# Optimization experiments

Measured on AMD Instinct MI355X. Metric: run time of the kernel, lower is better.

Reference implementation:

```python
import jax, jax.numpy as jnp
import numpy as np

N, E, D, L, RBF = 20000, 320000, 128, 3, 64
CUTOFF = 5.0
LN_EPS = 1e-5


def setup_inputs() -> dict:
    key = jax.random.key(0)
    ks = jax.random.split(key, 20)
    s = 0.05
    inp = {
        'z': jax.random.normal(ks[0], (N, 64), jnp.float32),
        'pos': jax.random.normal(ks[1], (N, 3), jnp.float32),
        'edge_index': jax.random.randint(ks[2], (2, E), 0, N),
        'in_w': jax.random.normal(ks[3], (64, D), jnp.float32) * s,
        'in_b': jnp.zeros((D,), jnp.float32),
        'filt_w': jax.random.normal(ks[4], (RBF, 3 * D), jnp.float32) * s,
        'filt_b': jnp.zeros((3 * D,), jnp.float32),
        'inter_w1': jax.random.normal(ks[5], (L, D, D), jnp.float32) * s,
        'inter_b1': jnp.zeros((L, D), jnp.float32),
        'inter_w2': jax.random.normal(ks[6], (L, D, 3 * D), jnp.float32) * s,
        'inter_b2': jnp.zeros((L, 3 * D), jnp.float32),
        'mix_mu_w': jax.random.normal(ks[7], (L, D, 2 * D), jnp.float32) * s,
        'mix_w1': jax.random.normal(ks[8], (L, 2 * D, D), jnp.float32) * s,
        'mix_b1': jnp.zeros((L, D), jnp.float32),
        'mix_w2': jax.random.normal(ks[9], (L, D, 3 * D), jnp.float32) * s,
        'mix_b2': jnp.zeros((L, 3 * D), jnp.float32),
        'mu_proj_w': jnp.zeros((D,), jnp.float32),  # nn.init.constant_(0.0) in source
        'ln_g': jnp.ones((D,), jnp.float32),
        'ln_b': jnp.zeros((D,), jnp.float32),
    }
    return inp


def painn_forward(z, pos, in_w, in_b, filt_w, filt_b, inter_w1, inter_b1,
                  inter_w2, inter_b2, mix_mu_w, mix_w1, mix_b1, mix_w2, mix_b2,
                  mu_proj_w, ln_g, ln_b, edge_index):
    idx_i, idx_j = edge_index[0], edge_index[1]
    # edge geometry
    r_ij = pos[idx_j] - pos[idx_i]                               # [E,3]
    d_ij = jnp.maximum(jnp.linalg.norm(r_ij, axis=1, keepdims=True), 1e-8)  # [E,1]
    dir_ij = r_ij / d_ij                                          # [E,3]
    # gaussian smearing
    offset = jnp.linspace(0.0, CUTOFF, RBF).astype(jnp.float32)
    coeff = -0.5 / (offset[1] - offset[0]) ** 2
    phi = jnp.exp(coeff * (d_ij - offset) ** 2)                   # [E,RBF]
    # cosine cutoff
    xc = jnp.clip(d_ij / CUTOFF, 0.0, 1.0)
    fcut = 0.5 * (jnp.cos(jnp.pi * xc) + 1.0) * (xc < 1.0)        # [E,1]
    filters = (phi @ filt_w + filt_b) * fcut                      # [E,3D]
    filters = jnp.clip(jnp.nan_to_num(filters), -5.0, 5.0)
    Wij = filters[:, None, :]                                     # [E,1,3D]

    q = jax.nn.silu(z @ in_w + in_b)[:, None, :]                  # [N,1,D]
    mu = jnp.zeros((N, 3, D), q.dtype)                            # [N,3,D]

    for l in range(L):
        # interaction (edge gather -> gate -> scatter-add)
        x = jax.nn.silu(q @ inter_w1[l] + inter_b1[l]) @ inter_w2[l] + inter_b2[l]  # [N,1,3D]
        xj = x[idx_j] * Wij                                       # [E,1,3D]
        dq, dmuR, dmumu = jnp.split(xj, 3, axis=-1)               # each [E,1,D]
        muj = mu[idx_j]                                           # [E,3,D]
        q = q + jax.ops.segment_sum(dq, idx_i, num_segments=N)
        dmu = dmuR * dir_ij[:, :, None] + dmumu * muj             # [E,3,D]
        mu = mu + jax.ops.segment_sum(dmu, idx_i, num_segments=N)
        # intra-atomic mixing
        mu_mix = mu @ mix_mu_w[l]                                  # [N,3,2D]
        mu_V, mu_W = jnp.split(mu_mix, 2, axis=-1)                 # [N,3,D]
        mu_Vn = jnp.sqrt(jnp.sum(mu_V ** 2, axis=-2, keepdims=True) + 1e-8)  # [N,1,D]
        ctx = jnp.concatenate([q, mu_Vn], axis=-1)                 # [N,1,2D]
        xm = jax.nn.silu(ctx @ mix_w1[l] + mix_b1[l]) @ mix_w2[l] + mix_b2[l]  # [N,1,3D]
        dq_i, dmu_i, dqmu_i = jnp.split(xm, 3, axis=-1)
        q = q + dq_i + dqmu_i * jnp.sum(mu_V * mu_W, axis=1, keepdims=True)
        mu = mu + dmu_i * mu_W

    node_attr = jnp.clip(jnp.nan_to_num(q[:, 0, :]), -5.0, 5.0)   # [N,D]
    mean = jnp.mean(node_attr, axis=-1, keepdims=True)
    var = jnp.var(node_attr, axis=-1, keepdims=True)
    node_attr = (node_attr - mean) * jax.lax.rsqrt(var + LN_EPS) * ln_g + ln_b
    node_attr = jnp.nan_to_num(jnp.tanh(node_attr))

    mu = jnp.nan_to_num(mu)
    mu_node = jax.ops.segment_sum(mu[idx_j], idx_i, num_segments=N)  # [N,3,D]
    mu_node = jnp.clip(jnp.nan_to_num(mu_node), -5.0, 5.0)
    pos_attr = jnp.clip(jnp.nan_to_num(mu_node @ mu_proj_w), -5.0, 5.0)  # [N,3]
    return node_attr, pos_attr


def reference(z, pos, edge_index, in_w, in_b, filt_w, filt_b, inter_w1, inter_b1,
              inter_w2, inter_b2, mix_mu_w, mix_w1, mix_b1, mix_w2, mix_b2,
              mu_proj_w, ln_g, ln_b):
    return painn_forward(z, pos, in_w, in_b, filt_w, filt_b, inter_w1, inter_b1,
                         inter_w2, inter_b2, mix_mu_w, mix_w1, mix_b1, mix_w2,
                         mix_b2, mu_proj_w, ln_g, ln_b, edge_index)
```

## Files before the change

kernel.cpp:

```cpp
#include <hip/hip_runtime.h>
#include <math.h>

#ifndef M_PI
#define M_PI 3.14159265358979323846
#endif

static constexpr int N_NODES = 20000;
static constexpr int N_EDGES = 320000;
static constexpr int NLAYER  = 3;
static constexpr int NB_SCAN = (N_NODES + 255) / 256;
static constexpr int TAB_T   = 1024;

typedef _Float16 f16;
typedef __attribute__((ext_vector_type(2))) _Float16 f16x2;
typedef __attribute__((ext_vector_type(8))) _Float16 f16x8;
typedef __attribute__((ext_vector_type(4))) float f32x4;

__global__ void k_hist(const int* __restrict__ idx_i, int* __restrict__ cnt) {
  int e = blockIdx.x * 256 + threadIdx.x;
  if (e < N_EDGES) atomicAdd(&cnt[idx_i[e]], 1);
}

__global__ void k_scan_blk(const int* __restrict__ cnt, int* __restrict__ incl,
                           int* __restrict__ bsum) {
  __shared__ int buf[256];
  int t = threadIdx.x;
  int i = blockIdx.x * 256 + t;
  int v = (i < N_NODES) ? cnt[i] : 0;
  buf[t] = v;
  __syncthreads();
  #pragma unroll
  for (int off = 1; off < 256; off <<= 1) {
    int x = (t >= off) ? buf[t - off] : 0;
    __syncthreads();
    buf[t] += x;
    __syncthreads();
  }
  if (i < N_NODES) incl[i] = buf[t];
  if (t == 255) bsum[blockIdx.x] = buf[255];
}

__global__ void k_scan_top(int* __restrict__ bsum) {
  __shared__ int buf[128];
  int t = threadIdx.x;
  int v = (t < NB_SCAN) ? bsum[t] : 0;
  buf[t] = v;
  __syncthreads();
  #pragma unroll
  for (int off = 1; off < 128; off <<= 1) {
    int x = (t >= off) ? buf[t - off] : 0;
    __syncthreads();
    buf[t] += x;
    __syncthreads();
  }
  if (t <= NB_SCAN) bsum[t] = buf[t] - v;
}

__global__ void k_scan_add(const int* __restrict__ cnt, const int* __restrict__ incl,
                           const int* __restrict__ bsum, int* __restrict__ rs,
                           int* __restrict__ cur) {
  int i = blockIdx.x * 256 + threadIdx.x;
  if (i < N_NODES) {
    int v = bsum[blockIdx.x] + incl[i] - cnt[i];
    rs[i] = v;
    cur[i] = v;
  }
  if (i == 0) rs[N_NODES] = bsum[NB_SCAN];
}

__global__ void k_fill_geom(const int* __restrict__ idx_all, const float* __restrict__ pos,
                            int* __restrict__ cur, float4* __restrict__ geo,
                            int* __restrict__ jperm) {
  int e = blockIdx.x * 256 + threadIdx.x;
  if (e >= N_EDGES) return;
  int i = idx_all[e];
  int j = idx_all[N_EDGES + e];
  int p = atomicAdd(&cur[i], 1);
  float rx = pos[j*3+0] - pos[i*3+0];
  float ry = pos[j*3+1] - pos[i*3+1];
  float rz = pos[j*3+2] - pos[i*3+2];
  float d = sqrtf(rx*rx + ry*ry + rz*rz);
  d = fmaxf(d, 1e-8f);
  float inv = 1.0f / d;
  geo[p] = make_float4(d, rx*inv, ry*inv, rz*inv);
  jperm[p] = j;
}

struct WJob { const float* src; f16* dst; int kshift; int ld; int col0; int nk; };
struct WJobs { WJob j[16]; };

__global__ __launch_bounds__(256) void k_prep(WJobs jb, const float* __restrict__ filt_w,
                                              const float* __restrict__ filt_b,
                                              f16* __restrict__ tab) {
  if (blockIdx.y < 16) {
    WJob w = jb.j[blockIdx.y];
    int t = blockIdx.x * 256 + threadIdx.x;
    if (t >= w.nk) return;
    int K = 1 << w.kshift;
    int n = t >> w.kshift;
    int k = t & (K - 1);
    w.dst[t] = (f16)w.src[(size_t)k * w.ld + w.col0 + n];
    return;
  }
  if (blockIdx.x >= 128) return;
  const int t = (blockIdx.y - 16) * 128 + blockIdx.x;
  __shared__ float ph[64];
  const int tid = threadIdx.x;
  const float dist = 5.0f * (float)t / (float)(TAB_T - 1);
  const float delta = 5.0f / 63.0f;
  const float coeff = -0.5f / (delta * delta);
  if (tid < 64) {
    float u = dist - delta * (float)tid;
    ph[tid] = expf(coeff * u * u);
  }
  __syncthreads();
  float xc = dist * 0.2f;
  float fc = (xc < 1.0f) ? 0.5f * (cosf((float)M_PI * xc) + 1.0f) : 0.0f;
  for (int n = tid; n < 384; n += 256) {
    float acc = 0.f;
    #pragma unroll
    for (int k = 0; k < 64; ++k) acc += ph[k] * filt_w[k * 384 + n];
    float v = (acc + filt_b[n]) * fc;
    v = fminf(fmaxf(v, -5.0f), 5.0f);
    tab[(size_t)t * 384 + n] = (f16)v;
  }
}

__global__ __launch_bounds__(256) void k_embed_i(
    const float* __restrict__ z, const f16* __restrict__ Win, const float* __restrict__ bin,
    const f16* __restrict__ Wi1, const float* __restrict__ bi1,
    const f16* __restrict__ Wi2, const float* __restrict__ bi2,
    float* __restrict__ q, f16* __restrict__ xout) {
  __shared__ __align__(16) char pool[16896];
  f16* QS  = (f16*)pool;
  f16* H2S = (f16*)(pool + 8448);
  const int tid = threadIdx.x;
  const int wave = tid >> 6, lane = tid & 63;
  const int lr = lane & 15, lk = lane >> 4;
  const int wmB = (wave & 1) * 16, wnB = (wave >> 1) * 64;
  const int n0 = blockIdx.x * 32;

  f32x4 accP[4] = {};
  #pragma unroll
  for (int kk = 0; kk < 2; ++kk) {
    const float* zp = z + (size_t)(n0 + wmB + lr) * 64 + kk * 32 + lk * 8;
    float4 v0 = ((const float4*)zp)[0];
    float4 v1 = ((const float4*)zp)[1];
    f16x8 af;
    af[0]=(f16)v0.x; af[1]=(f16)v0.y; af[2]=(f16)v0.z; af[3]=(f16)v0.w;
    af[4]=(f16)v1.x; af[5]=(f16)v1.y; af[6]=(f16)v1.z; af[7]=(f16)v1.w;
    f16x8 bf[4];
    #pragma unroll
    for (int nt = 0; nt < 4; ++nt)
      bf[nt] = *(const f16x8*)&Win[(size_t)(wnB + nt * 16 + lr) * 64 + kk * 32 + lk * 8];
    #pragma unroll
    for (int nt = 0; nt < 4; ++nt)
      accP[nt] = __builtin_amdgcn_mfma_f32_16x16x32_f16(af, bf[nt], accP[nt], 0, 0, 0);
  }
  #pragma unroll
  for (int nt = 0; nt < 4; ++nt) {
    int col = wnB + nt * 16 + lr;
    float bv = bin[col];
    #pragma unroll
    for (int rr = 0; rr < 4; ++rr) {
      int row = wmB + lk * 4 + rr;
      float v = accP[nt][rr] + bv;
      v = v / (1.0f + expf(-v));
      q[(size_t)(n0 + row) * 128 + col] = v;
      QS[row * 132 + col] = (f16)v;
    }
  }
  __syncthreads();

  f32x4 accD[4] = {};
  #pragma unroll
  for (int kk = 0; kk < 4; ++kk) {
    f16x8 af = *(const f16x8*)&QS[(wmB + lr) * 132 + kk * 32 + lk * 8];
    f16x8 bf[4];
    #pragma unroll
    for (int nt = 0; nt < 4; ++nt)
      bf[nt] = *(const f16x8*)&Wi1[(size_t)(wnB + nt * 16 + lr) * 128 + kk * 32 + lk * 8];
    #pragma unroll
    for (int nt = 0; nt < 4; ++nt)
      accD[nt] = __builtin_amdgcn_mfma_f32_16x16x32_f16(af, bf[nt], accD[nt], 0, 0, 0);
  }
  #pragma unroll
  for (int nt = 0; nt < 4; ++nt) {
    int col = wnB + nt * 16 + lr;
    float bv = bi1[col];
    #pragma unroll
    for (int rr = 0; rr < 4; ++rr) {
      int row = wmB + lk * 4 + rr;
      float v = accD[nt][rr] + bv;
      v = v / (1.0f + expf(-v));
      H2S[row * 132 + col] = (f16)v;
    }
  }
  __syncthreads();

  #pragma unroll
  for (int cc = 0; cc < 3; ++cc) {
    f32x4 accE[4] = {};
    #pragma unroll
    for (int kk = 0; kk < 4; ++kk) {
      f16x8 af = *(const f16x8*)&H2S[(wmB + lr) * 132 + kk * 32 + lk * 8];
      f16x8 bf[4];
      #pragma unroll
      for (int nt = 0; nt < 4; ++nt)
        bf[nt] = *(const f16x8*)&Wi2[(size_t)(cc * 128 + wnB + nt * 16 + lr) * 128 + kk * 32 + lk * 8];
      #pragma unroll
      for (int nt = 0; nt < 4; ++nt)
        accE[nt] = __builtin_amdgcn_mfma_f32_16x16x32_f16(af, bf[nt], accE[nt], 0, 0, 0);
    }
    #pragma unroll
    for (int nt = 0; nt < 4; ++nt) {
      int gn = cc * 128 + wnB + nt * 16 + lr;
      float bv = bi2[gn];
      #pragma unroll
      for (int rr = 0; rr < 4; ++rr) {
        int gm = n0 + wmB + lk * 4 + rr;
        xout[(size_t)gm * 384 + gn] = (f16)(accE[nt][rr] + bv);
      }
    }
  }
}

template<int MODE>
__global__ __launch_bounds__(256) void k_mix(
    float* __restrict__ q, f16* __restrict__ mu,
    const f16* __restrict__ Wmu,
    const f16* __restrict__ W1, const float* __restrict__ b1,
    const f16* __restrict__ W2, const float* __restrict__ b2,
    const f16* __restrict__ Wi1, const float* __restrict__ bi1,
    const f16* __restrict__ Wi2, const float* __restrict__ bi2,
    f16* __restrict__ xout,
    const float* __restrict__ ln_g, const float* __restrict__ ln_b,
    float* __restrict__ out_node) {
  __shared__ __align__(16) char pool[50688 + 25344];
  f16*   MM  = (f16*)pool;
  char*  scr = pool + 50688;
  f16*   As4 = (f16*)scr;
  f16*   VN  = (f16*)scr;
  f16*   HS  = (f16*)(scr + 8448);
  f16*   QS  = (f16*)(scr + 16896);
  f16*   H2S = (f16*)scr;
  float* QSf = (float*)scr;

  const int tid = threadIdx.x;
  const int wave = tid >> 6, lane = tid & 63;
  const int lr = lane & 15, lk = lane >> 4;
  const int n0 = blockIdx.x * 32;
  const int r0 = n0 * 3;

  #pragma unroll
  for (int rep = 0; rep < 6; ++rep) {
    int idx = rep * 256 + tid;
    int row = idx >> 4;
    int g   = idx & 15;
    int kb = g >> 2, c8 = g & 3;
    f16x8 v = *(const f16x8*)(mu + (size_t)(r0 + row) * 128 + g * 8);
    *(f16x8*)&As4[((kb * 96 + row) << 5) + ((c8 ^ ((row >> 1) & 3)) << 3)] = v;
  }
  __syncthreads();

  const int wmA = (wave & 1) * 48;
  const int wnA0 = (wave >> 1) * 64;
  #pragma unroll
  for (int half = 0; half < 2; ++half) {
    f32x4 accA[3][4] = {};
    #pragma unroll
    for (int kk = 0; kk < 4; ++kk) {
      f16x8 af[3], bf[4];
      #pragma unroll
      for (int mt = 0; mt < 3; ++mt) {
        int r = wmA + mt * 16 + lr;
        af[mt] = *(const f16x8*)&As4[((kk * 96 + r) << 5) + ((lk ^ ((r >> 1) & 3)) << 3)];
      }
      #pragma unroll
      for (int nt = 0; nt < 4; ++nt)
        bf[nt] = *(const f16x8*)&Wmu[(size_t)(half * 128 + wnA0 + nt * 16 + lr) * 128 + kk * 32 + lk * 8];
      #pragma unroll
      for (int mt = 0; mt < 3; ++mt)
        #pragma unroll
        for (int nt = 0; nt < 4; ++nt)
          accA[mt][nt] = __builtin_amdgcn_mfma_f32_16x16x32_f16(af[mt], bf[nt], accA[mt][nt], 0, 0, 0);
    }
    #pragma unroll
    for (int mt = 0; mt < 3; ++mt)
      #pragma unroll
      for (int nt = 0; nt < 4; ++nt) {
        int col = half * 128 + wnA0 + nt * 16 + lr;
        #pragma unroll
        for (int rr = 0; rr < 4; ++rr) {
          int row = wmA + mt * 16 + lk * 4 + rr;
          MM[row * 264 + col] = (f16)accA[mt][nt][rr];
        }
      }
  }
  __syncthreads();

  #pragma unroll
  for (int rep = 0; rep < 16; ++rep) {
    int idx = rep * 256 + tid;
    int nn = idx >> 7, c = idx & 127;
    float V0 = (float)MM[(nn * 3 + 0) * 264 + c];
    float V1 = (float)MM[(nn * 3 + 1) * 264 + c];
    float V2 = (float)MM[(nn * 3 + 2) * 264 + c];
    float vnv = sqrtf(V0 * V0 + V1 * V1 + V2 * V2 + 1e-8f);
    int kb = c >> 5, c8 = (c >> 3) & 3, ce = c & 7;
    VN[((kb * 32 + nn) << 5) + ((c8 ^ ((nn >> 1) & 3)) << 3) + ce] = (f16)vnv;
  }
  __syncthreads();

  const int wmB = (wave & 1) * 16, wnB = (wave >> 1) * 64;
  f32x4 accB[4] = {};
  #pragma unroll
  for (int kk = 0; kk < 8; ++kk) {
    f16x8 af;
    int row = wmB + lr;
    if (kk < 4) {
      const float* qp_ = q + (size_t)(n0 + row) * 128 + kk * 32 + lk * 8;
      float4 v0 = ((const float4*)qp_)[0];
      float4 v1 = ((const float4*)qp_)[1];
      af[0]=(f16)v0.x; af[1]=(f16)v0.y; af[2]=(f16)v0.z; af[3]=(f16)v0.w;
      af[4]=(f16)v1.x; af[5]=(f16)v1.y; af[6]=(f16)v1.z; af[7]=(f16)v1.w;
    } else {
      af = *(const f16x8*)&VN[(((kk - 4) * 32 + row) << 5) + ((lk ^ ((row >> 1) & 3)) << 3)];
    }
    f16x8 bf[4];
    #pragma unroll
    for (int nt = 0; nt < 4; ++nt)
      bf[nt] = *(const f16x8*)&W1[(size_t)(wnB + nt * 16 + lr) * 256 + kk * 32 + lk * 8];
    #pragma unroll
    for (int nt = 0; nt < 4; ++nt)
      accB[nt] = __builtin_amdgcn_mfma_f32_16x16x32_f16(af, bf[nt], accB[nt], 0, 0, 0);
  }
  #pragma unroll
  for (int nt = 0; nt < 4; ++nt) {
    int col = wnB + nt * 16 + lr;
    float bv = b1[col];
    #pragma unroll
    for (int rr = 0; rr < 4; ++rr) {
      int row = wmB + lk * 4 + rr;
      float v = accB[nt][rr] + bv;
      v = v / (1.0f + expf(-v));
      HS[row * 132 + col] = (f16)v;
    }
  }
  __syncthreads();

  f32x4 accC[3][4] = {};
  #pragma unroll
  for (int cc = 0; cc < 3; ++cc)
    #pragma unroll
    for (int kk = 0; kk < 4; ++kk) {
      f16x8 af = *(const f16x8*)&HS[(wmB + lr) * 132 + kk * 32 + lk * 8];
      f16x8 bf[4];
      #pragma unroll
      for (int nt = 0; nt < 4; ++nt)
        bf[nt] = *(const f16x8*)&W2[(size_t)(cc * 128 + wnB + nt * 16 + lr) * 128 + kk * 32 + lk * 8];
      #pragma unroll
      for (int nt = 0; nt < 4; ++nt)
        accC[cc][nt] = __builtin_amdgcn_mfma_f32_16x16x32_f16(af, bf[nt], accC[cc][nt], 0, 0, 0);
    }
  __syncthreads();

  #pragma unroll
  for (int nt = 0; nt < 4; ++nt) {
    int col = wnB + nt * 16 + lr;
    float b_dq = b2[col], b_dmu = b2[128 + col], b_dqmu = b2[256 + col];
    #pragma unroll
    for (int rr = 0; rr < 4; ++rr) {
      int nn = wmB + lk * 4 + rr;
      int gm = n0 + nn;
      float dq   = accC[0][nt][rr] + b_dq;
      float dmu  = accC[1][nt][rr] + b_dmu;
      float dqmu = accC[2][nt][rr] + b_dqmu;
      float V0 = (float)MM[(nn * 3 + 0) * 264 + col], W0 = (float)MM[(nn * 3 + 0) * 264 + 128 + col];
      float V1 = (float)MM[(nn * 3 + 1) * 264 + col], W1v = (float)MM[(nn * 3 + 1) * 264 + 128 + col];
      float V2 = (float)MM[(nn * 3 + 2) * 264 + col], W2v = (float)MM[(nn * 3 + 2) * 264 + 128 + col];
      float svw = V0 * W0 + V1 * W1v + V2 * W2v;
      size_t qi = (size_t)gm * 128 + col;
      float qnew = q[qi] + dq + dqmu * svw;
      if constexpr (MODE == 0) {
        q[qi] = qnew;
        QS[nn * 132 + col] = (f16)qnew;
      } else {
        QSf[nn * 132 + col] = qnew;
      }
      f16* mr = mu + (size_t)gm * 384;
      mr[col]       = (f16)((float)mr[col]       + dmu * W0);
      mr[128 + col] = (f16)((float)mr[128 + col] + dmu * W1v);
      mr[256 + col] = (f16)((float)mr[256 + col] + dmu * W2v);
    }
  }
  __syncthreads();

  if constexpr (MODE == 0) {
    f32x4 accD[4] = {};
    #pragma unroll
    for (int kk = 0; kk < 4; ++kk) {
      f16x8 af = *(const f16x8*)&QS[(wmB + lr) * 132 + kk * 32 + lk * 8];
      f16x8 bf[4];
      #pragma unroll
      for (int nt = 0; nt < 4; ++nt)
        bf[nt] = *(const f16x8*)&Wi1[(size_t)(wnB + nt * 16 + lr) * 128 + kk * 32 + lk * 8];
      #pragma unroll
      for (int nt = 0; nt < 4; ++nt)
        accD[nt] = __builtin_amdgcn_mfma_f32_16x16x32_f16(af, bf[nt], accD[nt], 0, 0, 0);
    }
    #pragma unroll
    for (int nt = 0; nt < 4; ++nt) {
      int col = wnB + nt * 16 + lr;
      float bv = bi1[col];
      #pragma unroll
      for (int rr = 0; rr < 4; ++rr) {
        int row = wmB + lk * 4 + rr;
        float v = accD[nt][rr] + bv;
        v = v / (1.0f + expf(-v));
        H2S[row * 132 + col] = (f16)v;
      }
    }
    __syncthreads();
    #pragma unroll
    for (int cc = 0; cc < 3; ++cc) {
      f32x4 accE[4] = {};
      #pragma unroll
      for (int kk = 0; kk < 4; ++kk) {
        f16x8 af = *(const f16x8*)&H2S[(wmB + lr) * 132 + kk * 32 + lk * 8];
        f16x8 bf[4];
        #pragma unroll
        for (int nt = 0; nt < 4; ++nt)
          bf[nt] = *(const f16x8*)&Wi2[(size_t)(cc * 128 + wnB + nt * 16 + lr) * 128 + kk * 32 + lk * 8];
        #pragma unroll
        for (int nt = 0; nt < 4; ++nt)
          accE[nt] = __builtin_amdgcn_mfma_f32_16x16x32_f16(af, bf[nt], accE[nt], 0, 0, 0);
      }
      #pragma unroll
      for (int nt = 0; nt < 4; ++nt) {
        int gn = cc * 128 + wnB + nt * 16 + lr;
        float bv = bi2[gn];
        #pragma unroll
        for (int rr = 0; rr < 4; ++rr) {
          int gm = n0 + wmB + lk * 4 + rr;
          xout[(size_t)gm * 384 + gn] = (f16)(accE[nt][rr] + bv);
        }
      }
    }
  } else {
    const int d0 = lane * 2;
    #pragma unroll
    for (int rr2 = 0; rr2 < 8; ++rr2) {
      int nn = wave * 8 + rr2;
      float v0 = QSf[nn * 132 + d0];
      float v1 = QSf[nn * 132 + d0 + 1];
      v0 = fminf(fmaxf(v0, -5.f), 5.f);
      v1 = fminf(fmaxf(v1, -5.f), 5.f);
      float s = v0 + v1, s2 = v0 * v0 + v1 * v1;
      #pragma unroll
      for (int off = 32; off > 0; off >>= 1) {
        s  += __shfl_down(s,  off, 64);
        s2 += __shfl_down(s2, off, 64);
      }
      s  = __shfl(s,  0, 64);
      s2 = __shfl(s2, 0, 64);
      float mean = s * (1.0f / 128.0f);
      float var  = s2 * (1.0f / 128.0f) - mean * mean;
      float r = rsqrtf(var + 1e-5f);
      size_t o = (size_t)(n0 + nn) * 128 + d0;
      out_node[o]     = tanhf((v0 - mean) * r * ln_g[d0]     + ln_b[d0]);
      out_node[o + 1] = tanhf((v1 - mean) * r * ln_g[d0 + 1] + ln_b[d0 + 1]);
    }
  }
}

template<bool HASMU>
__global__ __launch_bounds__(256) void k_edge_msg(
    const int* __restrict__ rs, const int* __restrict__ jperm,
    const f16* __restrict__ x, const f16* __restrict__ tab,
    const float4* __restrict__ geo, const f16* __restrict__ mu_in,
    float* __restrict__ q, f16* __restrict__ mu_out) {
  const int wid  = threadIdx.x >> 6;
  const int lane = threadIdx.x & 63;
  const int i = blockIdx.x * 4 + wid;
  if (i >= N_NODES) return;
  const int d0 = lane * 2;
  const float scale = (float)(TAB_T - 1) / 5.0f;
  float aqx = 0.f, aqy = 0.f;
  float a0x = 0.f, a0y = 0.f, a1x = 0.f, a1y = 0.f, a2x = 0.f, a2y = 0.f;
  const int s = rs[i], e = rs[i + 1];

  for (int p = s; p < e; ++p) {
    int j = jperm[p];
    float4 g = geo[p];
    float u = fminf(g.x, 5.0f) * scale;
    int t0 = min((int)u, TAB_T - 2);
    float fr = u - (float)t0, fo = 1.0f - fr;
    const f16* ta = tab + (size_t)t0 * 384;
    const f16* xj = x + (size_t)j * 384;
    f16x2 ta0 = *(const f16x2*)(ta + d0);
    f16x2 ta1 = *(const f16x2*)(ta + 128 + d0);
    f16x2 tb0 = *(const f16x2*)(ta + 384 + d0);
    f16x2 tb1 = *(const f16x2*)(ta + 512 + d0);
    f16x2 xv0 = *(const f16x2*)(xj + d0);
    f16x2 xv1 = *(const f16x2*)(xj + 128 + d0);
    float W0x = fo * (float)ta0[0] + fr * (float)tb0[0];
    float W0y = fo * (float)ta0[1] + fr * (float)tb0[1];
    float W1x = fo * (float)ta1[0] + fr * (float)tb1[0];
    float W1y = fo * (float)ta1[1] + fr * (float)tb1[1];
    float m1x = (float)xv1[0] * W1x, m1y = (float)xv1[1] * W1y;
    aqx = fmaf((float)xv0[0], W0x, aqx);
    aqy = fmaf((float)xv0[1], W0y, aqy);
    if constexpr (HASMU) {
      f16x2 ta2 = *(const f16x2*)(ta + 256 + d0);
      f16x2 tb2 = *(const f16x2*)(ta + 640 + d0);
      f16x2 xv2 = *(const f16x2*)(xj + 256 + d0);
      const f16* mj = mu_in + (size_t)j * 384;
      f16x2 mv0 = *(const f16x2*)(mj + d0);
      f16x2 mv1 = *(const f16x2*)(mj + 128 + d0);
      f16x2 mv2 = *(const f16x2*)(mj + 256 + d0);
      float W2x = fo * (float)ta2[0] + fr * (float)tb2[0];
      float W2y = fo * (float)ta2[1] + fr * (float)tb2[1];
      float m2x = (float)xv2[0] * W2x, m2y = (float)xv2[1] * W2y;
      a0x += m1x * g.y + m2x * (float)mv0[0];
      a0y += m1y * g.y + m2y * (float)mv0[1];
      a1x += m1x * g.z + m2x * (float)mv1[0];
      a1y += m1y * g.z + m2y * (float)mv1[1];
      a2x += m1x * g.w + m2x * (float)mv2[0];
      a2y += m1y * g.w + m2y * (float)mv2[1];
    } else {
      a0x += m1x * g.y; a0y += m1y * g.y;
      a1x += m1x * g.z; a1y += m1y * g.z;
      a2x += m1x * g.w; a2y += m1y * g.w;
    }
  }

  float* qp = q + (size_t)i * 128 + d0;
  float2 qv = *(float2*)qp;
  qv.x += aqx; qv.y += aqy;
  *(float2*)qp = qv;
  f16* mout = mu_out + (size_t)i * 384;
  f16x2 o0, o1, o2;
  if constexpr (HASMU) {
    const f16* min_ = mu_in + (size_t)i * 384;
    f16x2 i0 = *(const f16x2*)(min_ + d0);
    f16x2 i1 = *(const f16x2*)(min_ + 128 + d0);
    f16x2 i2 = *(const f16x2*)(min_ + 256 + d0);
    o0[0] = (f16)((float)i0[0] + a0x); o0[1] = (f16)((float)i0[1] + a0y);
    o1[0] = (f16)((float)i1[0] + a1x); o1[1] = (f16)((float)i1[1] + a1y);
    o2[0] = (f16)((float)i2[0] + a2x); o2[1] = (f16)((float)i2[1] + a2y);
  } else {
    o0[0] = (f16)a0x; o0[1] = (f16)a0y;
    o1[0] = (f16)a1x; o1[1] = (f16)a1y;
    o2[0] = (f16)a2x; o2[1] = (f16)a2y;
  }
  *(f16x2*)(mout + d0)       = o0;
  *(f16x2*)(mout + 128 + d0) = o1;
  *(f16x2*)(mout + 256 + d0) = o2;
}

__global__ __launch_bounds__(256) void k_posattr(
    const int* __restrict__ rs, const int* __restrict__ jperm,
    const f16* __restrict__ mu, const float* __restrict__ w, float* __restrict__ pos_out) {
  const int wid  = threadIdx.x >> 6;
  const int lane = threadIdx.x & 63;
  const int i = blockIdx.x * 4 + wid;
  if (i >= N_NODES) return;
  const int d0 = lane * 2;
  float a0x = 0.f, a0y = 0.f, a1x = 0.f, a1y = 0.f, a2x = 0.f, a2y = 0.f;
  float wx = w[d0], wy = w[d0 + 1];
  if (wx != 0.0f || wy != 0.0f) {
    const int s = rs[i], e = rs[i + 1];
    for (int p = s; p < e; ++p) {
      int j = jperm[p];
      const f16* mj = mu + (size_t)j * 384;
      f16x2 A0 = *(const f16x2*)(mj + d0);
      f16x2 A1 = *(const f16x2*)(mj + 128 + d0);
      f16x2 A2 = *(const f16x2*)(mj + 256 + d0);
      a0x += (float)A0[0]; a0y += (float)A0[1];
      a1x += (float)A1[0]; a1y += (float)A1[1];
      a2x += (float)A2[0]; a2y += (float)A2[1];
    }
  }
  float s0 = fminf(fmaxf(a0x, -5.f), 5.f) * wx + fminf(fmaxf(a0y, -5.f), 5.f) * wy;
  float s1 = fminf(fmaxf(a1x, -5.f), 5.f) * wx + fminf(fmaxf(a1y, -5.f), 5.f) * wy;
  float s2 = fminf(fmaxf(a2x, -5.f), 5.f) * wx + fminf(fmaxf(a2y, -5.f), 5.f) * wy;
  #pragma unroll
  for (int off = 32; off > 0; off >>= 1) {
    s0 += __shfl_down(s0, off, 64);
    s1 += __shfl_down(s1, off, 64);
    s2 += __shfl_down(s2, off, 64);
  }
  if (lane == 0) {
    pos_out[(size_t)i * 3 + 0] = fminf(fmaxf(s0, -5.f), 5.f);
    pos_out[(size_t)i * 3 + 1] = fminf(fmaxf(s1, -5.f), 5.f);
    pos_out[(size_t)i * 3 + 2] = fminf(fmaxf(s2, -5.f), 5.f);
  }
}

extern "C" void kernel_launch(void* const* d_in, const int* in_sizes, int n_in,
                              void* d_out, int out_size, void* d_ws, size_t ws_size,
                              hipStream_t stream) {
  const float* z         = (const float*)d_in[0];
  const float* pos       = (const float*)d_in[1];
  const int*   edge_idx  = (const int*)d_in[2];
  const float* in_w      = (const float*)d_in[3];
  const float* in_b      = (const float*)d_in[4];
  const float* filt_w    = (const float*)d_in[5];
  const float* filt_b    = (const float*)d_in[6];
  const float* inter_w1  = (const float*)d_in[7];
  const float* inter_b1  = (const float*)d_in[8];
  const float* inter_w2  = (const float*)d_in[9];
  const float* inter_b2  = (const float*)d_in[10];
  const float* mix_mu_w  = (const float*)d_in[11];
  const float* mix_w1    = (const float*)d_in[12];
  const float* mix_b1    = (const float*)d_in[13];
  const float* mix_w2    = (const float*)d_in[14];
  const float* mix_b2    = (const float*)d_in[15];
  const float* mu_proj_w = (const float*)d_in[16];
  const float* ln_g      = (const float*)d_in[17];
  const float* ln_b      = (const float*)d_in[18];

  char* base = (char*)d_ws;
  size_t off = 0;
  auto alloc = [&](size_t bytes) -> char* {
    char* p = base + off;
    off += (bytes + 255) & ~(size_t)255;
    return p;
  };
  float*  q     = (float*)alloc((size_t)N_NODES * 128 * 4);
  f16*    x16   = (f16*)alloc((size_t)N_NODES * 384 * 2);
  f16*    mu_a  = (f16*)alloc((size_t)N_NODES * 384 * 2);
  f16*    mu_b  = (f16*)alloc((size_t)N_NODES * 384 * 2);
  float4* geo   = (float4*)alloc((size_t)N_EDGES * 16);
  int*    cnt   = (int*)alloc((size_t)N_NODES * 4);
  int*    incl  = (int*)alloc((size_t)N_NODES * 4);
  int*    bsum  = (int*)alloc(128 * 4);
  int*    rs    = (int*)alloc((size_t)(N_NODES + 1) * 4);
  int*    cur   = (int*)alloc((size_t)N_NODES * 4);
  int*    jperm = (int*)alloc((size_t)N_EDGES * 4);
  f16*    tab   = (f16*)alloc((size_t)TAB_T * 384 * 2);
  f16* wt_in = (f16*)alloc((size_t)128 * 64 * 2);
  f16* wt_i1 = (f16*)alloc((size_t)3 * 128 * 128 * 2);
  f16* wt_i2 = (f16*)alloc((size_t)3 * 384 * 128 * 2);
  f16* wt_mu = (f16*)alloc((size_t)3 * 256 * 128 * 2);
  f16* wt_x1 = (f16*)alloc((size_t)3 * 128 * 256 * 2);
  f16* wt_x2 = (f16*)alloc((size_t)3 * 384 * 128 * 2);
  if (off > ws_size) return;

  float* out_node = (float*)d_out;
  float* out_pos  = (float*)d_out + (size_t)N_NODES * 128;

  {
    WJobs jb;
    int ji = 0;
    jb.j[ji++] = {in_w, wt_in, 6, 128, 0, 128 * 64};
    for (int l = 0; l < 3; ++l)
      jb.j[ji++] = {inter_w1 + (size_t)l*128*128, wt_i1 + (size_t)l*128*128, 7, 128, 0, 128*128};
    for (int l = 0; l < 3; ++l)
      jb.j[ji++] = {inter_w2 + (size_t)l*128*384, wt_i2 + (size_t)l*384*128, 7, 384, 0, 384*128};
    for (int l = 0; l < 3; ++l)
      jb.j[ji++] = {mix_mu_w + (size_t)l*128*256, wt_mu + (size_t)l*256*128, 7, 256, 0, 256*128};
    for (int l = 0; l < 3; ++l)
      jb.j[ji++] = {mix_w1 + (size_t)l*256*128, wt_x1 + (size_t)l*128*256, 8, 128, 0, 128*256};
    for (int l = 0; l < 3; ++l)
      jb.j[ji++] = {mix_w2 + (size_t)l*128*384, wt_x2 + (size_t)l*384*128, 7, 384, 0, 384*128};
    dim3 g(192, 24);
    k_prep<<<g, 256, 0, stream>>>(jb, filt_w, filt_b, tab);
  }

  hipMemsetAsync(cnt, 0, (size_t)N_NODES * 4, stream);
  k_hist<<<N_EDGES / 256, 256, 0, stream>>>(edge_idx, cnt);
  k_scan_blk<<<NB_SCAN, 256, 0, stream>>>(cnt, incl, bsum);
  k_scan_top<<<1, 128, 0, stream>>>(bsum);
  k_scan_add<<<NB_SCAN, 256, 0, stream>>>(cnt, incl, bsum, rs, cur);
  k_fill_geom<<<N_EDGES / 256, 256, 0, stream>>>(edge_idx, pos, cur, geo, jperm);

  const int gmx = N_NODES / 32;
  const int gn4 = (N_NODES + 3) / 4;
  k_embed_i<<<gmx, 256, 0, stream>>>(z, wt_in, in_b,
                                     wt_i1, inter_b1, wt_i2, inter_b2, q, x16);

  f16* mu_cur = mu_a;
  f16* mu_nxt = mu_b;
  for (int l = 0; l < NLAYER; ++l) {
    if (l == 0)
      k_edge_msg<false><<<gn4, 256, 0, stream>>>(rs, jperm, x16, tab, geo, mu_cur, q, mu_nxt);
    else
      k_edge_msg<true><<<gn4, 256, 0, stream>>>(rs, jperm, x16, tab, geo, mu_cur, q, mu_nxt);
    { f16* t = mu_cur; mu_cur = mu_nxt; mu_nxt = t; }
    if (l < NLAYER - 1) {
      k_mix<0><<<gmx, 256, 0, stream>>>(q, mu_cur, wt_mu + (size_t)l*256*128,
                                        wt_x1 + (size_t)l*128*256, mix_b1 + (size_t)l*128,
                                        wt_x2 + (size_t)l*384*128, mix_b2 + (size_t)l*384,
                                        wt_i1 + (size_t)(l+1)*128*128, inter_b1 + (size_t)(l+1)*128,
                                        wt_i2 + (size_t)(l+1)*384*128, inter_b2 + (size_t)(l+1)*384,
                                        x16, nullptr, nullptr, nullptr);
    } else {
      k_mix<1><<<gmx, 256, 0, stream>>>(q, mu_cur, wt_mu + (size_t)l*256*128,
                                        wt_x1 + (size_t)l*128*256, mix_b1 + (size_t)l*128,
                                        wt_x2 + (size_t)l*384*128, mix_b2 + (size_t)l*384,
                                        nullptr, nullptr, nullptr, nullptr, nullptr,
                                        ln_g, ln_b, out_node);
    }
  }

  k_posattr<<<gn4, 256, 0, stream>>>(rs, jperm, mu_cur, mu_proj_w, out_pos);
}
```

Measured before the change: 546.3 us.

## Restructure k_mix mu projection to keep V/W in registers, shrink LDS

The k_mix kernel no longer stages mu in swizzled LDS or writes the full V/W projection matrix to shared memory. Each wave now loads its mu rows straight from global and computes the V and W projections for all three spatial components in registers. It derives the vector norm, the W components and the V·W dot product per lane, then writes only the norm to LDS. This cuts LDS from about 76KB to 25KB and removes two sync/staging passes, with launch bounds raised to 3 blocks per CU for more occupancy. The cost is many more live accumulator registers (24 f32x4), which risks register pressure or spills under the new occupancy bound.

After: 573.6 us. 5.0% more time.

```diff
diff --git a/kernel.cpp b/kernel.cpp
--- a/kernel.cpp
+++ b/kernel.cpp
@@ -137,13 +137,13 @@
   const int tid = threadIdx.x;
   const int wave = tid >> 6, lane = tid & 63;
   const int lr = lane & 15, lk = lane >> 4;
-  const int wmB = (wave & 1) * 16, wnB = (wave >> 1) * 64;
+  const int wm = (wave & 1) * 16, wn = (wave >> 1) * 64;
   const int n0 = blockIdx.x * 32;
 
   f32x4 accP[4] = {};
   #pragma unroll
   for (int kk = 0; kk < 2; ++kk) {
-    const float* zp = z + (size_t)(n0 + wmB + lr) * 64 + kk * 32 + lk * 8;
+    const float* zp = z + (size_t)(n0 + wm + lr) * 64 + kk * 32 + lk * 8;
     float4 v0 = ((const float4*)zp)[0];
     float4 v1 = ((const float4*)zp)[1];
     f16x8 af;
@@ -152,18 +152,18 @@
     f16x8 bf[4];
     #pragma unroll
     for (int nt = 0; nt < 4; ++nt)
-      bf[nt] = *(const f16x8*)&Win[(size_t)(wnB + nt * 16 + lr) * 64 + kk * 32 + lk * 8];
+      bf[nt] = *(const f16x8*)&Win[(size_t)(wn + nt * 16 + lr) * 64 + kk * 32 + lk * 8];
     #pragma unroll
     for (int nt = 0; nt < 4; ++nt)
       accP[nt] = __builtin_amdgcn_mfma_f32_16x16x32_f16(af, bf[nt], accP[nt], 0, 0, 0);
   }
   #pragma unroll
   for (int nt = 0; nt < 4; ++nt) {
-    int col = wnB + nt * 16 + lr;
+    int col = wn + nt * 16 + lr;
     float bv = bin[col];
     #pragma unroll
     for (int rr = 0; rr < 4; ++rr) {
-      int row = wmB + lk * 4 + rr;
+      int row = wm + lk * 4 + rr;
       float v = accP[nt][rr] + bv;
       v = v / (1.0f + expf(-v));
       q[(size_t)(n0 + row) * 128 + col] = v;
@@ -175,22 +175,22 @@
   f32x4 accD[4] = {};
   #pragma unroll
   for (int kk = 0; kk < 4; ++kk) {
-    f16x8 af = *(const f16x8*)&QS[(wmB + lr) * 132 + kk * 32 + lk * 8];
+    f16x8 af = *(const f16x8*)&QS[(wm + lr) * 132 + kk * 32 + lk * 8];
     f16x8 bf[4];
     #pragma unroll
     for (int nt = 0; nt < 4; ++nt)
-      bf[nt] = *(const f16x8*)&Wi1[(size_t)(wnB + nt * 16 + lr) * 128 + kk * 32 + lk * 8];
+      bf[nt] = *(const f16x8*)&Wi1[(size_t)(wn + nt * 16 + lr) * 128 + kk * 32 + lk * 8];
     #pragma unroll
     for (int nt = 0; nt < 4; ++nt)
       accD[nt] = __builtin_amdgcn_mfma_f32_16x16x32_f16(af, bf[nt], accD[nt], 0, 0, 0);
   }
   #pragma unroll
   for (int nt = 0; nt < 4; ++nt) {
-    int col = wnB + nt * 16 + lr;
+    int col = wn + nt * 16 + lr;
     float bv = bi1[col];
     #pragma unroll
     for (int rr = 0; rr < 4; ++rr) {
-      int row = wmB + lk * 4 + rr;
+      int row = wm + lk * 4 + rr;
       float v = accD[nt][rr] + bv;
       v = v / (1.0f + expf(-v));
       H2S[row * 132 + col] = (f16)v;
@@ -203,22 +203,22 @@
     f32x4 accE[4] = {};
     #pragma unroll
     for (int kk = 0; kk < 4; ++kk) {
-      f16x8 af = *(const f16x8*)&H2S[(wmB + lr) * 132 + kk * 32 + lk * 8];
+      f16x8 af = *(const f16x8*)&H2S[(wm + lr) * 132 + kk * 32 + lk * 8];
       f16x8 bf[4];
       #pragma unroll
       for (int nt = 0; nt < 4; ++nt)
-        bf[nt] = *(const f16x8*)&Wi2[(size_t)(cc * 128 + wnB + nt * 16 + lr) * 128 + kk * 32 + lk * 8];
+        bf[nt] = *(const f16x8*)&Wi2[(size_t)(cc * 128 + wn + nt * 16 + lr) * 128 + kk * 32 + lk * 8];
       #pragma unroll
       for (int nt = 0; nt < 4; ++nt)
         accE[nt] = __builtin_amdgcn_mfma_f32_16x16x32_f16(af, bf[nt], accE[nt], 0, 0, 0);
     }
     #pragma unroll
     for (int nt = 0; nt < 4; ++nt) {
-      int gn = cc * 128 + wnB + nt * 16 + lr;
+      int gn = cc * 128 + wn + nt * 16 + lr;
       float bv = bi2[gn];
       #pragma unroll
       for (int rr = 0; rr < 4; ++rr) {
-        int gm = n0 + wmB + lk * 4 + rr;
+        int gm = n0 + wm + lk * 4 + rr;
         xout[(size_t)gm * 384 + gn] = (f16)(accE[nt][rr] + bv);
       }
     }
@@ -226,7 +226,7 @@
 }
 
 template<int MODE>
-__global__ __launch_bounds__(256) void k_mix(
+__global__ __launch_bounds__(256, 3) void k_mix(
     float* __restrict__ q, f16* __restrict__ mu,
     const f16* __restrict__ Wmu,
     const f16* __restrict__ W1, const float* __restrict__ b1,
@@ -236,115 +236,83 @@
     f16* __restrict__ xout,
     const float* __restrict__ ln_g, const float* __restrict__ ln_b,
     float* __restrict__ out_node) {
-  __shared__ __align__(16) char pool[50688 + 25344];
-  f16*   MM  = (f16*)pool;
-  char*  scr = pool + 50688;
-  f16*   As4 = (f16*)scr;
-  f16*   VN  = (f16*)scr;
-  f16*   HS  = (f16*)(scr + 8448);
-  f16*   QS  = (f16*)(scr + 16896);
-  f16*   H2S = (f16*)scr;
-  float* QSf = (float*)scr;
+  __shared__ __align__(16) char pool[25344];
+  f16*   VN  = (f16*)pool;
+  f16*   HS  = (f16*)(pool + 8448);
+  f16*   QS  = (f16*)(pool + 16896);
+  f16*   H2S = (f16*)pool;
+  float* QSf = (float*)(pool + 8448);
 
   const int tid = threadIdx.x;
   const int wave = tid >> 6, lane = tid & 63;
   const int lr = lane & 15, lk = lane >> 4;
+  const int wm = (wave & 1) * 16;
+  const int wn = (wave >> 1) * 64;
   const int n0 = blockIdx.x * 32;
-  const int r0 = n0 * 3;
-
-  #pragma unroll
-  for (int rep = 0; rep < 6; ++rep) {
-    int idx = rep * 256 + tid;
-    int row = idx >> 4;
-    int g   = idx & 15;
-    int kb = g >> 2, c8 = g & 3;
-    f16x8 v = *(const f16x8*)(mu + (size_t)(r0 + row) * 128 + g * 8);
-    *(f16x8*)&As4[((kb * 96 + row) << 5) + ((c8 ^ ((row >> 1) & 3)) << 3)] = v;
-  }
-  __syncthreads();
-
-  const int wmA = (wave & 1) * 48;
-  const int wnA0 = (wave >> 1) * 64;
-  #pragma unroll
-  for (int half = 0; half < 2; ++half) {
-    f32x4 accA[3][4] = {};
-    #pragma unroll
-    for (int kk = 0; kk < 4; ++kk) {
-      f16x8 af[3], bf[4];
+
+  f32x4 accV[3][4] = {};
+  f32x4 accW[3][4] = {};
+  #pragma unroll
+  for (int kk = 0; kk < 4; ++kk) {
+    f16x8 af[3];
+    #pragma unroll
+    for (int mt = 0; mt < 3; ++mt)
+      af[mt] = *(const f16x8*)(mu + (size_t)(n0 + wm + lr) * 384 + mt * 128 + kk * 32 + lk * 8);
+    #pragma unroll
+    for (int nt = 0; nt < 4; ++nt) {
+      f16x8 bfV = *(const f16x8*)&Wmu[(size_t)(wn + nt * 16 + lr) * 128 + kk * 32 + lk * 8];
+      f16x8 bfW = *(const f16x8*)&Wmu[(size_t)(128 + wn + nt * 16 + lr) * 128 + kk * 32 + lk * 8];
       #pragma unroll
       for (int mt = 0; mt < 3; ++mt) {
-        int r = wmA + mt * 16 + lr;
-        af[mt] = *(const f16x8*)&As4[((kk * 96 + r) << 5) + ((lk ^ ((r >> 1) & 3)) << 3)];
+        accV[mt][nt] = __builtin_amdgcn_mfma_f32_16x16x32_f16(af[mt], bfV, accV[mt][nt], 0, 0, 0);
+        accW[mt][nt] = __builtin_amdgcn_mfma_f32_16x16x32_f16(af[mt], bfW, accW[mt][nt], 0, 0, 0);
       }
-      #pragma unroll
-      for (int nt = 0; nt < 4; ++nt)
-        bf[nt] = *(const f16x8*)&Wmu[(size_t)(half * 128 + wnA0 + nt * 16 + lr) * 128 + kk * 32 + lk * 8];
-      #pragma unroll
-      for (int mt = 0; mt < 3; ++mt)
-        #pragma unroll
-        for (int nt = 0; nt < 4; ++nt)
-          accA[mt][nt] = __builtin_amdgcn_mfma_f32_16x16x32_f16(af[mt], bf[nt], accA[mt][nt], 0, 0, 0);
-    }
-    #pragma unroll
-    for (int mt = 0; mt < 3; ++mt)
-      #pragma unroll
-      for (int nt = 0; nt < 4; ++nt) {
-        int col = half * 128 + wnA0 + nt * 16 + lr;
-        #pragma unroll
-        for (int rr = 0; rr < 4; ++rr) {
-          int row = wmA + mt * 16 + lk * 4 + rr;
-          MM[row * 264 + col] = (f16)accA[mt][nt][rr];
-        }
-      }
-  }
-  __syncthreads();
-
-  #pragma unroll
-  for (int rep = 0; rep < 16; ++rep) {
-    int idx = rep * 256 + tid;
-    int nn = idx >> 7, c = idx & 127;
-    float V0 = (float)MM[(nn * 3 + 0) * 264 + c];
-    float V1 = (float)MM[(nn * 3 + 1) * 264 + c];
-    float V2 = (float)MM[(nn * 3 + 2) * 264 + c];
-    float vnv = sqrtf(V0 * V0 + V1 * V1 + V2 * V2 + 1e-8f);
-    int kb = c >> 5, c8 = (c >> 3) & 3, ce = c & 7;
-    VN[((kb * 32 + nn) << 5) + ((c8 ^ ((nn >> 1) & 3)) << 3) + ce] = (f16)vnv;
-  }
-  __syncthreads();
-
-  const int wmB = (wave & 1) * 16, wnB = (wave >> 1) * 64;
+    }
+  }
+  f16 Wp0[4][4], Wp1[4][4], Wp2[4][4], svp[4][4];
+  #pragma unroll
+  for (int nt = 0; nt < 4; ++nt)
+    #pragma unroll
+    for (int rr = 0; rr < 4; ++rr) {
+      float V0 = accV[0][nt][rr], V1 = accV[1][nt][rr], V2 = accV[2][nt][rr];
+      float W0 = accW[0][nt][rr], W1v = accW[1][nt][rr], W2v = accW[2][nt][rr];
+      Wp0[nt][rr] = (f16)W0; Wp1[nt][rr] = (f16)W1v; Wp2[nt][rr] = (f16)W2v;
+      svp[nt][rr] = (f16)(V0 * W0 + V1 * W1v + V2 * W2v);
+      float vnv = sqrtf(V0 * V0 + V1 * V1 + V2 * V2 + 1e-8f);
+      VN[(wm + lk * 4 + rr) * 132 + wn + nt * 16 + lr] = (f16)vnv;
+    }
+  __syncthreads();
+
   f32x4 accB[4] = {};
   #pragma unroll
   for (int kk = 0; kk < 8; ++kk) {
     f16x8 af;
-    int row = wmB + lr;
     if (kk < 4) {
-      const float* qp_ = q + (size_t)(n0 + row) * 128 + kk * 32 + lk * 8;
+      const float* qp_ = q + (size_t)(n0 + wm + lr) * 128 + kk * 32 + lk * 8;
       float4 v0 = ((const float4*)qp_)[0];
       float4 v1 = ((const float4*)qp_)[1];
       af[0]=(f16)v0.x; af[1]=(f16)v0.y; af[2]=(f16)v0.z; af[3]=(f16)v0.w;
       af[4]=(f16)v1.x; af[5]=(f16)v1.y; af[6]=(f16)v1.z; af[7]=(f16)v1.w;
     } else {
-      af = *(const f16x8*)&VN[(((kk - 4) * 32 + row) << 5) + ((lk ^ ((row >> 1) & 3)) << 3)];
+      af = *(const f16x8*)&VN[(wm + lr) * 132 + (kk - 4) * 32 + lk * 8];
     }
     f16x8 bf[4];
     #pragma unroll
     for (int nt = 0; nt < 4; ++nt)
-      bf[nt] = *(const f16x8*)&W1[(size_t)(wnB + nt * 16 + lr) * 256 + kk * 32 + lk * 8];
+      bf[nt] = *(const f16x8*)&W1[(size_t)(wn + nt * 16 + lr) * 256 + kk * 32 + lk * 8];
     #pragma unroll
     for (int nt = 0; nt < 4; ++nt)
       accB[nt] = __builtin_amdgcn_mfma_f32_16x16x32_f16(af, bf[nt], accB[nt], 0, 0, 0);
   }
   #pragma unroll
   for (int nt = 0; nt < 4; ++nt) {
-    int col = wnB + nt * 16 + lr;
+    int col = wn + nt * 16 + lr;
     float bv = b1[col];
     #pragma unroll
     for (int rr = 0; rr < 4; ++rr) {
-      int row = wmB + lk * 4 + rr;
       float v = accB[nt][rr] + bv;
       v = v / (1.0f + expf(-v));
-      HS[row * 132 + col] = (f16)v;
+      HS[(wm + lk * 4 + rr) * 132 + col] = (f16)v;
     }
   }
   __syncthreads();
@@ -354,11 +322,11 @@
   for (int cc = 0; cc < 3; ++cc)
     #pragma unroll
     for (int kk = 0; kk < 4; ++kk) {
-      f16x8 af = *(const f16x8*)&HS[(wmB + lr) * 132 + kk * 32 + lk * 8];
+      f16x8 af = *(const f16x8*)&HS[(wm + lr) * 132 + kk * 32 + lk * 8];
       f16x8 bf[4];
       #pragma unroll
       for (int nt = 0; nt < 4; ++nt)
-        bf[nt] = *(const f16x8*)&W2[(size_t)(cc * 128 + wnB + nt * 16 + lr) * 128 + kk * 32 + lk * 8];
+        bf[nt] = *(const f16x8*)&W2[(size_t)(cc * 128 + wn + nt * 16 + lr) * 128 + kk * 32 + lk * 8];
       #pragma unroll
       for (int nt = 0; nt < 4; ++nt)
         accC[cc][nt] = __builtin_amdgcn_mfma_f32_16x16x32_f16(af, bf[nt], accC[cc][nt], 0, 0, 0);
@@ -367,21 +335,18 @@
 
   #pragma unroll
   for (int nt = 0; nt < 4; ++nt) {
-    int col = wnB + nt * 16 + lr;
+    int col = wn + nt * 16 + lr;
     float b_dq = b2[col], b_dmu = b2[128 + col], b_dqmu = b2[256 + col];
     #pragma unroll
     for (int rr = 0; rr < 4; ++rr) {
-      int nn = wmB + lk * 4 + rr;
+      int nn = wm + lk * 4 + rr;
       int gm = n0 + nn;
       float dq   = accC[0][nt][rr] + b_dq;
       float dmu  = accC[1][nt][rr] + b_dmu;
       float dqmu = accC[2][nt][rr] + b_dqmu;
-      float V0 = (float)MM[(nn * 3 + 0) * 264 + col], W0 = (float)MM[(nn * 3 + 0) * 264 + 128 + col];
-      float V1 = (float)MM[(nn * 3 + 1) * 264 + col], W1v = (float)MM[(nn * 3 + 1) * 264 + 128 + col];
-      float V2 = (float)MM[(nn * 3 + 2) * 264 + col], W2v = (float)MM[(nn * 3 + 2) * 264 + 128 + col];
-      float svw = V0 * W0 + V1 * W1v + V2 * W2v;
+      float W0 = (float)Wp0[nt][rr], W1v = (float)Wp1[nt][rr], W2v = (float)Wp2[nt][rr];
       size_t qi = (size_t)gm * 128 + col;
-      float qnew = q[qi] + dq + dqmu * svw;
+      float qnew = q[qi] + dq + dqmu * (float)svp[nt][rr];
       if constexpr (MODE == 0) {
         q[qi] = qnew;
         QS[nn * 132 + col] = (f16)qnew;
@@ -400,25 +365,24 @@
     f32x4 accD[4] = {};
     #pragma unroll
     for (int kk = 0; kk < 4; ++kk) {
-      f16x8 af = *(const f16x8*)&QS[(wmB + lr) * 132 + kk * 32 + lk * 8];
+      f16x8 af = *(const f16x8*)&QS[(wm + lr) * 132 + kk * 32 + lk * 8];
       f16x8 bf[4];
       #pragma unroll
       for (int nt = 0; nt < 4; ++nt)
-        bf[nt] = *(const f16x8*)&Wi1[(size_t)(wnB + nt * 16 + lr) * 128 + kk * 32 + lk * 8];
+        bf[nt] = *(const f16x8*)&Wi1[(size_t)(wn + nt * 16 + lr) * 128 + kk * 32 + lk * 8];
       #pragma unroll
       for (int nt = 0; nt < 4; ++nt)
         accD[nt] = __builtin_amdgcn_mfma_f32_16x16x32_f16(af, bf[nt], accD[nt], 0, 0, 0);
     }
     #pragma unroll
     for (int nt = 0; nt < 4; ++nt) {
-      int col = wnB + nt * 16 + lr;
+      int col = wn + nt * 16 + lr;
       float bv = bi1[col];
       #pragma unroll
       for (int rr = 0; rr < 4; ++rr) {
-        int row = wmB + lk * 4 + rr;
         float v = accD[nt][rr] + bv;
         v = v / (1.0f + expf(-v));
-        H2S[row * 132 + col] = (f16)v;
+        H2S[(wm + lk * 4 + rr) * 132 + col] = (f16)v;
       }
     }
     __syncthreads();
@@ -427,22 +391,22 @@
       f32x4 accE[4] = {};
       #pragma unroll
       for (int kk = 0; kk < 4; ++kk) {
-        f16x8 af = *(const f16x8*)&H2S[(wmB + lr) * 132 + kk * 32 + lk * 8];
+        f16x8 af = *(const f16x8*)&H2S[(wm + lr) * 132 + kk * 32 + lk * 8];
         f16x8 bf[4];
         #pragma unroll
         for (int nt = 0; nt < 4; ++nt)
-          bf[nt] = *(const f16x8*)&Wi2[(size_t)(cc * 128 + wnB + nt * 16 + lr) * 128 + kk * 32 + lk * 8];
+          bf[nt] = *(const f16x8*)&Wi2[(size_t)(cc * 128 + wn + nt * 16 + lr) * 128 + kk * 32 + lk * 8];
         #pragma unroll
         for (int nt = 0; nt < 4; ++nt)
           accE[nt] = __builtin_amdgcn_mfma_f32_16x16x32_f16(af, bf[nt], accE[nt], 0, 0, 0);
       }
       #pragma unroll
       for (int nt = 0; nt < 4; ++nt) {
-        int gn = cc * 128 + wnB + nt * 16 + lr;
+        int gn = cc * 128 + wn + nt * 16 + lr;
         float bv = bi2[gn];
         #pragma unroll
         for (int rr = 0; rr < 4; ++rr) {
-          int gm = n0 + wmB + lk * 4 + rr;
+          int gm = n0 + wm + lk * 4 + rr;
           xout[(size_t)gm * 384 + gn] = (f16)(accE[nt][rr] + bv);
         }
       }
```
